# Kernel tuning notes

Hardware: AMD Instinct MI355X
Metric: run time of the kernel (lower is better)

Reference implementation:

```python
import jax, jax.numpy as jnp
import numpy as np

B, L, H, Dh, M = 4, 2048, 16, 256, 1024
D = H * Dh  # 4096

def setup_inputs() -> dict:
    key = jax.random.key(0)
    kx, ku, kd, kp = jax.random.split(key, 4)
    x = jax.random.normal(kx, (B, L, D), dtype=jnp.float32)
    up = jax.random.normal(ku, (H, Dh, M), dtype=jnp.float32)
    down = jax.random.normal(kd, (H, M, Dh), dtype=jnp.float32)
    perm = jax.random.permutation(kp, D)  # int32/int64 permutation of feature dim
    return {"x": x, "up": up, "down": down, "perm": perm}

def reference(x, up, down, perm):
    b, l, Dm = x.shape
    h, d = up.shape[0], up.shape[1]
    unperm = jnp.argsort(perm)  # inverse permutation (Unpermute buffer)
    t = x.reshape(b * l, Dm)
    t = t[:, perm]                     # PermuteIn gather
    t = t.reshape(b * l, h, d)
    t = jnp.einsum('bhd,hdm->bhm', t, up)      # per-head up-proj (grouped GEMM)
    t = jax.nn.gelu(t, approximate=False)      # nn.GELU default = exact erf
    t = jnp.einsum('bhm,hmd->bhd', t, down)    # per-head down-proj
    t = t.reshape(b * l, h * d)
    t = t[:, unperm]                   # Unpermute gather
    out = t.reshape(b, l, Dm)
    # residual=False: self.residual(x, residual) returns x (computed output)
    return out
```

## Files before the change

### kernel.cpp

```cpp
#include <hip/hip_runtime.h>
#include <hip/hip_bf16.h>
#include <math.h>


typedef __attribute__((ext_vector_type(8))) short bf16x8;
typedef __attribute__((ext_vector_type(4))) float f32x4;

__device__ __forceinline__ unsigned short f2bf(float f) {
    unsigned int u = __builtin_bit_cast(unsigned int, f);
    u = (u + 0x7FFFu + ((u >> 16) & 1u)) >> 16;
    return (unsigned short)u;
}
__device__ __forceinline__ float bf2f(unsigned short u) {
    return __builtin_bit_cast(float, ((unsigned int)u) << 16);
}

__device__ __forceinline__ float gelu_fast(float x) {
    float x2 = x * x;
    float a = x * __builtin_fmaf(-0.10294437f, x2, -2.3022082f);
    return x * __builtin_amdgcn_rcpf(1.0f + __builtin_amdgcn_exp2f(a));
}

__global__ __launch_bounds__(256) void transpose_cvt_kernel(
        const float* __restrict__ src, unsigned short* __restrict__ dst,
        int R, int C) {
    int tilesC = C >> 6;
    int tiles = tilesC * (R >> 6);
    int h = blockIdx.x / tiles;
    int t = blockIdx.x % tiles;
    int r0 = (t / tilesC) << 6;
    int c0 = (t % tilesC) << 6;
    const float* s = src + (size_t)h * R * C;
    unsigned short* d = dst + (size_t)h * R * C;
    __shared__ float tl[64][65];
    int col = threadIdx.x & 63;
    int rr = threadIdx.x >> 6;
    #pragma unroll
    for (int i = 0; i < 16; ++i) {
        int row = (i << 2) + rr;
        tl[row][col] = s[(size_t)(r0 + row) * C + (c0 + col)];
    }
    __syncthreads();
    #pragma unroll
    for (int i = 0; i < 16; ++i) {
        int row = (i << 2) + rr;
        d[(size_t)(c0 + row) * R + (r0 + col)] = f2bf(tl[col][row]);
    }
}

__global__ __launch_bounds__(256) void permute_x_kernel(
        const float* __restrict__ x, const int* __restrict__ perm,
        unsigned short* __restrict__ xP) {
    __shared__ unsigned short rbf[4][4096];
    __shared__ int sperm[4096];
    int tid = threadIdx.x;
    #pragma unroll
    for (int i = 0; i < 16; ++i) sperm[(i << 8) + tid] = perm[(i << 8) + tid];
    size_t r0 = (size_t)blockIdx.x << 2;
    #pragma unroll
    for (int rr = 0; rr < 4; ++rr) {
        const float4* xr = (const float4*)(x + ((r0 + rr) << 12));
        #pragma unroll
        for (int i = 0; i < 4; ++i) {
            float4 v = xr[(i << 8) + tid];
            int j = ((i << 8) + tid) << 2;
            uint2 wv;
            wv.x = f2bf(v.x) | ((unsigned int)f2bf(v.y) << 16);
            wv.y = f2bf(v.z) | ((unsigned int)f2bf(v.w) << 16);
            *(uint2*)(&rbf[rr][j]) = wv;
        }
    }
    __syncthreads();
    #pragma unroll
    for (int rr = 0; rr < 4; ++rr) {
        alignas(16) unsigned short tmp[16];
        int j0 = tid << 4;
        #pragma unroll
        for (int i = 0; i < 16; ++i) tmp[i] = rbf[rr][sperm[j0 + i]];
        *(uint4*)(xP + ((r0 + rr) << 12) + j0) = *(const uint4*)tmp;
        *(uint4*)(xP + ((r0 + rr) << 12) + j0 + 8) = *(const uint4*)(tmp + 8);
    }
}

template<int F32>
__global__ __launch_bounds__(256) void unpermute_kernel(
        const void* __restrict__ yPv, const int* __restrict__ perm,
        float* __restrict__ out) {
    __shared__ float rows[4][4096];
    __shared__ int sperm[4096];
    int tid = threadIdx.x;
    #pragma unroll
    for (int i = 0; i < 16; ++i) sperm[(i << 8) + tid] = perm[(i << 8) + tid];
    size_t r0 = (size_t)blockIdx.x << 2;
    int j0 = tid << 4;
    float vals[4][16];
    #pragma unroll
    for (int rr = 0; rr < 4; ++rr) {
        if (F32) {
            const float4* yr = (const float4*)((const float*)yPv + ((r0 + rr) << 12) + j0);
            #pragma unroll
            for (int i = 0; i < 4; ++i) {
                float4 v = yr[i];
                vals[rr][4 * i] = v.x; vals[rr][4 * i + 1] = v.y;
                vals[rr][4 * i + 2] = v.z; vals[rr][4 * i + 3] = v.w;
            }
        } else {
            const uint2* yr = (const uint2*)((const unsigned short*)yPv + ((r0 + rr) << 12) + j0);
            #pragma unroll
            for (int i = 0; i < 4; ++i) {
                uint2 v = yr[i];
                vals[rr][4 * i]     = bf2f((unsigned short)(v.x & 0xffffu));
                vals[rr][4 * i + 1] = bf2f((unsigned short)(v.x >> 16));
                vals[rr][4 * i + 2] = bf2f((unsigned short)(v.y & 0xffffu));
                vals[rr][4 * i + 3] = bf2f((unsigned short)(v.y >> 16));
            }
        }
    }
    __syncthreads();
    #pragma unroll
    for (int rr = 0; rr < 4; ++rr)
        #pragma unroll
        for (int i = 0; i < 16; ++i)
            rows[rr][sperm[j0 + i]] = vals[rr][i];
    __syncthreads();
    #pragma unroll
    for (int rr = 0; rr < 4; ++rr) {
        float4* orow = (float4*)(out + ((r0 + rr) << 12));
        #pragma unroll
        for (int i = 0; i < 4; ++i)
            orow[(i << 8) + tid] = *(const float4*)(&rows[rr][((i << 8) + tid) << 2]);
    }
}

template<int YPF32>
__global__ __launch_bounds__(256, 3) void ffn_kernel(
    const unsigned short* __restrict__ xP,
    const unsigned short* __restrict__ upT,
    const unsigned short* __restrict__ downT,
    void* __restrict__ yPv)
{
    __shared__ unsigned char sA[64 * 512];
    __shared__ unsigned char sH[64 * 256];

    int tid = threadIdx.x;
    int lane = tid & 63;
    int wave = tid >> 6;
    int l15 = lane & 15;
    int lq = lane >> 4;

    int bid = blockIdx.x;
    int nb = ((bid & 7) << 8) + (bid >> 3);
    int head = nb >> 7;
    int row0 = (nb & 127) << 6;

    #pragma unroll
    for (int i = 0; i < 8; ++i) {
        int idx = tid + (i << 8);
        int r = idx >> 5;
        int s = idx & 31;
        const unsigned short* src = xP + (((size_t)(row0 + r)) << 12) + (head << 8) + (s << 3);
        bf16x8 v = *(const bf16x8*)src;
        *(bf16x8*)(sA + r * 512 + ((s ^ (r & 31)) << 4)) = v;
    }
    __syncthreads();

    int wr = wave & 1;
    int wm = wave >> 1;

    f32x4 acc[4][4] = {};

    for (int mc = 0; mc < 8; ++mc) {
        int m0 = mc << 7;

        f32x4 hacc[4][2] = {};
        #pragma unroll
        for (int ks = 0; ks < 8; ++ks) {
            bf16x8 xb[2];
            #pragma unroll
            for (int j = 0; j < 2; ++j) {
                int r = ((2 * wr + j) << 4) + l15;
                int bo = r * 512 + ((((ks << 6) + (lq << 4))) ^ ((r & 31) << 4));
                xb[j] = *(const bf16x8*)(sA + bo);
            }
            bf16x8 wf[4];
            int kk = (ks << 5) + (lq << 3);
            #pragma unroll
            for (int i = 0; i < 4; ++i) {
                int m = m0 + (((wm << 2) + i) << 4) + l15;
                wf[i] = *(const bf16x8*)(upT + ((size_t)((head << 10) + m) << 8) + kk);
            }
            __builtin_amdgcn_s_setprio(1);
            #pragma unroll
            for (int i = 0; i < 4; ++i)
                #pragma unroll
                for (int j = 0; j < 2; ++j)
                    hacc[i][j] = __builtin_amdgcn_mfma_f32_16x16x32_bf16(wf[i], xb[j], hacc[i][j], 0, 0, 0);
            __builtin_amdgcn_s_setprio(0);
        }
        #pragma unroll
        for (int i = 0; i < 4; ++i) {
            #pragma unroll
            for (int j = 0; j < 2; ++j) {
                int r = ((2 * wr + j) << 4) + l15;
                int mbyte = (((wm << 2) + i) << 5) + (lq << 3);
                float g0 = gelu_fast(hacc[i][j][0]);
                float g1 = gelu_fast(hacc[i][j][1]);
                float g2 = gelu_fast(hacc[i][j][2]);
                float g3 = gelu_fast(hacc[i][j][3]);
                uint2 wv;
                wv.x = f2bf(g0) | ((unsigned int)f2bf(g1) << 16);
                wv.y = f2bf(g2) | ((unsigned int)f2bf(g3) << 16);
                *(uint2*)(sH + r * 256 + (mbyte ^ ((r & 15) << 4))) = wv;
            }
        }
        __syncthreads();

        #pragma unroll
        for (int ks = 0; ks < 4; ++ks) {
            bf16x8 ha[4];
            #pragma unroll
            for (int rb = 0; rb < 4; ++rb) {
                int r = (rb << 4) + l15;
                int bo = r * 256 + ((((ks << 6) + (lq << 4))) ^ ((r & 15) << 4));
                ha[rb] = *(const bf16x8*)(sH + bo);
            }
            bf16x8 wf[4];
            int mg = m0 + (ks << 5) + (lq << 3);
            #pragma unroll
            for (int i = 0; i < 4; ++i) {
                int d = (((wave << 2) + i) << 4) + l15;
                wf[i] = *(const bf16x8*)(downT + ((size_t)((head << 8) + d) << 10) + mg);
            }
            __builtin_amdgcn_s_setprio(1);
            #pragma unroll
            for (int i = 0; i < 4; ++i)
                #pragma unroll
                for (int rb = 0; rb < 4; ++rb)
                    acc[rb][i] = __builtin_amdgcn_mfma_f32_16x16x32_bf16(ha[rb], wf[i], acc[rb][i], 0, 0, 0);
            __builtin_amdgcn_s_setprio(0);
        }
        __syncthreads();
    }

    if (YPF32) {
        float* yp = (float*)yPv;
        #pragma unroll
        for (int rb = 0; rb < 4; ++rb)
            #pragma unroll
            for (int i = 0; i < 4; ++i) {
                int rg = row0 + (rb << 4) + (lq << 2);
                int dc = (head << 8) + (((wave << 2) + i) << 4) + l15;
                #pragma unroll
                for (int e = 0; e < 4; ++e)
                    yp[((size_t)(rg + e) << 12) + dc] = acc[rb][i][e];
            }
    } else {
        unsigned short* yp = (unsigned short*)yPv;
        #pragma unroll
        for (int rb = 0; rb < 4; ++rb)
            #pragma unroll
            for (int i = 0; i < 4; ++i) {
                int rg = row0 + (rb << 4) + (lq << 2);
                int dc = (head << 8) + (((wave << 2) + i) << 4) + l15;
                #pragma unroll
                for (int e = 0; e < 4; ++e)
                    yp[((size_t)(rg + e) << 12) + dc] = f2bf(acc[rb][i][e]);
            }
    }
}

extern "C" void kernel_launch(void* const* d_in, const int* in_sizes, int n_in,
                              void* d_out, int out_size, void* d_ws, size_t ws_size,
                              hipStream_t stream) {
    const float* x    = (const float*)d_in[0];
    const float* up   = (const float*)d_in[1];
    const float* down = (const float*)d_in[2];
    const int*   perm = (const int*)d_in[3];
    float* out = (float*)d_out;

    const size_t W = (size_t)16 * 1024 * 256;
    const size_t XN = (size_t)8192 * 4096;
    unsigned short* upT   = (unsigned short*)d_ws;
    unsigned short* downT = upT + W;
    unsigned short* xP    = downT + W;
    void* yP = (void*)(xP + XN);
    size_t base_bytes = (2 * W + XN) * 2;
    bool ypf32 = ws_size >= base_bytes + XN * 4;

    transpose_cvt_kernel<<<16 * 4 * 16, 256, 0, stream>>>(up, upT, 256, 1024);
    transpose_cvt_kernel<<<16 * 16 * 4, 256, 0, stream>>>(down, downT, 1024, 256);
    permute_x_kernel<<<2048, 256, 0, stream>>>(x, perm, xP);

    if (ypf32) {
        ffn_kernel<1><<<2048, 256, 0, stream>>>(xP, upT, downT, yP);
        unpermute_kernel<1><<<2048, 256, 0, stream>>>(yP, perm, out);
    } else {
        ffn_kernel<0><<<2048, 256, 0, stream>>>(xP, upT, downT, yP);
        unpermute_kernel<0><<<2048, 256, 0, stream>>>(yP, perm, out);
    }
}
```

Baseline: 659.2 us.

## Register-prefetch up/down weight fragments and reassign waves to full row set

Reworks the fused up-proj/GELU/down-proj kernel so each wave computes 32 M-columns across all 64 rows instead of a 2x2 row/column split. This halves the global up-weight fragment loads per wave while doubling LDS reads of the activation tile. It also software-pipelines the global weight loads for both GEMMs, loading the next k-step's fragments into registers before issuing the current MFMAs, including across chunk boundaries and before the barrier. The aim is to hide global load latency behind MFMA work, at the cost of more live registers and possibly lower occupancy.

```diff
diff --git a/kernel.cpp b/kernel.cpp
--- a/kernel.cpp
+++ b/kernel.cpp
@@ -153,6 +153,9 @@
     int head = nb >> 7;
     int row0 = (nb & 127) << 6;
 
+    const unsigned short* upH = upT + ((size_t)head << 18);
+    const unsigned short* dnH = downT + ((size_t)head << 18);
+
     #pragma unroll
     for (int i = 0; i < 8; ++i) {
         int idx = tid + (i << 8);
@@ -164,55 +167,73 @@
     }
     __syncthreads();
 
-    int wr = wave & 1;
-    int wm = wave >> 1;
+    int mrow0 = (wave << 5) + l15;
+    int kk0 = lq << 3;
 
     f32x4 acc[4][4] = {};
+
+    bf16x8 w1n0, w1n1;
+    {
+        const unsigned short* p = upH + (size_t)mrow0 * 256 + kk0;
+        w1n0 = *(const bf16x8*)p;
+        w1n1 = *(const bf16x8*)(p + 16 * 256);
+    }
 
     for (int mc = 0; mc < 8; ++mc) {
         int m0 = mc << 7;
 
-        f32x4 hacc[4][2] = {};
+        f32x4 hacc[2][4] = {};
         #pragma unroll
         for (int ks = 0; ks < 8; ++ks) {
-            bf16x8 xb[2];
-            #pragma unroll
-            for (int j = 0; j < 2; ++j) {
-                int r = ((2 * wr + j) << 4) + l15;
-                int bo = r * 512 + ((((ks << 6) + (lq << 4))) ^ ((r & 31) << 4));
-                xb[j] = *(const bf16x8*)(sA + bo);
-            }
-            bf16x8 wf[4];
-            int kk = (ks << 5) + (lq << 3);
-            #pragma unroll
-            for (int i = 0; i < 4; ++i) {
-                int m = m0 + (((wm << 2) + i) << 4) + l15;
-                wf[i] = *(const bf16x8*)(upT + ((size_t)((head << 10) + m) << 8) + kk);
+            bf16x8 w1c0 = w1n0, w1c1 = w1n1;
+            {
+                int nks = (ks + 1) & 7;
+                int nm0 = (ks == 7) ? (((mc + 1) & 7) << 7) : m0;
+                const unsigned short* p = upH + (size_t)(nm0 + mrow0) * 256 + (nks << 5) + kk0;
+                w1n0 = *(const bf16x8*)p;
+                w1n1 = *(const bf16x8*)(p + 16 * 256);
+            }
+            bf16x8 xb[4];
+            #pragma unroll
+            for (int rb = 0; rb < 4; ++rb) {
+                int r = (rb << 4) + l15;
+                xb[rb] = *(const bf16x8*)(sA + r * 512 + (((ks << 6) + (lq << 4)) ^ ((r & 31) << 4)));
             }
             __builtin_amdgcn_s_setprio(1);
             #pragma unroll
-            for (int i = 0; i < 4; ++i)
-                #pragma unroll
-                for (int j = 0; j < 2; ++j)
-                    hacc[i][j] = __builtin_amdgcn_mfma_f32_16x16x32_bf16(wf[i], xb[j], hacc[i][j], 0, 0, 0);
+            for (int rb = 0; rb < 4; ++rb) {
+                hacc[0][rb] = __builtin_amdgcn_mfma_f32_16x16x32_bf16(w1c0, xb[rb], hacc[0][rb], 0, 0, 0);
+                hacc[1][rb] = __builtin_amdgcn_mfma_f32_16x16x32_bf16(w1c1, xb[rb], hacc[1][rb], 0, 0, 0);
+            }
             __builtin_amdgcn_s_setprio(0);
         }
-        #pragma unroll
-        for (int i = 0; i < 4; ++i) {
-            #pragma unroll
-            for (int j = 0; j < 2; ++j) {
-                int r = ((2 * wr + j) << 4) + l15;
-                int mbyte = (((wm << 2) + i) << 5) + (lq << 3);
-                float g0 = gelu_fast(hacc[i][j][0]);
-                float g1 = gelu_fast(hacc[i][j][1]);
-                float g2 = gelu_fast(hacc[i][j][2]);
-                float g3 = gelu_fast(hacc[i][j][3]);
+
+        #pragma unroll
+        for (int jm = 0; jm < 2; ++jm) {
+            int mbyte = (((wave << 1) + jm) << 5) + (lq << 3);
+            #pragma unroll
+            for (int rb = 0; rb < 4; ++rb) {
+                int r = (rb << 4) + l15;
+                float g0 = gelu_fast(hacc[jm][rb][0]);
+                float g1 = gelu_fast(hacc[jm][rb][1]);
+                float g2 = gelu_fast(hacc[jm][rb][2]);
+                float g3 = gelu_fast(hacc[jm][rb][3]);
                 uint2 wv;
                 wv.x = f2bf(g0) | ((unsigned int)f2bf(g1) << 16);
                 wv.y = f2bf(g2) | ((unsigned int)f2bf(g3) << 16);
                 *(uint2*)(sH + r * 256 + (mbyte ^ ((r & 15) << 4))) = wv;
             }
         }
+
+        bf16x8 wf2[4];
+        {
+            int mg = m0 + kk0;
+            #pragma unroll
+            for (int i = 0; i < 4; ++i) {
+                int d = (((wave << 2) + i) << 4) + l15;
+                wf2[i] = *(const bf16x8*)(dnH + (size_t)d * 1024 + mg);
+            }
+        }
         __syncthreads();
 
         #pragma unroll
@@ -221,22 +242,25 @@
             #pragma unroll
             for (int rb = 0; rb < 4; ++rb) {
                 int r = (rb << 4) + l15;
-                int bo = r * 256 + ((((ks << 6) + (lq << 4))) ^ ((r & 15) << 4));
-                ha[rb] = *(const bf16x8*)(sH + bo);
-            }
-            bf16x8 wf[4];
-            int mg = m0 + (ks << 5) + (lq << 3);
-            #pragma unroll
-            for (int i = 0; i < 4; ++i) {
-                int d = (((wave << 2) + i) << 4) + l15;
-                wf[i] = *(const bf16x8*)(downT + ((size_t)((head << 8) + d) << 10) + mg);
+                ha[rb] = *(const bf16x8*)(sH + r * 256 + (((ks << 6) + (lq << 4)) ^ ((r & 15) << 4)));
+            }
+            bf16x8 wcur[4];
+            #pragma unroll
+            for (int i = 0; i < 4; ++i) wcur[i] = wf2[i];
+            if (ks < 3) {
+                int mg = m0 + ((ks + 1) << 5) + kk0;
+                #pragma unroll
+                for (int i = 0; i < 4; ++i) {
+                    int d = (((wave << 2) + i) << 4) + l15;
+                    wf2[i] = *(const bf16x8*)(dnH + (size_t)d * 1024 + mg);
+                }
             }
             __builtin_amdgcn_s_setprio(1);
             #pragma unroll
             for (int i = 0; i < 4; ++i)
                 #pragma unroll
                 for (int rb = 0; rb < 4; ++rb)
-                    acc[rb][i] = __builtin_amdgcn_mfma_f32_16x16x32_bf16(ha[rb], wf[i], acc[rb][i], 0, 0, 0);
+                    acc[rb][i] = __builtin_amdgcn_mfma_f32_16x16x32_bf16(ha[rb], wcur[i], acc[rb][i], 0, 0, 0);
             __builtin_amdgcn_s_setprio(0);
         }
         __syncthreads();
```

New measurement: 561.9 us. -14.8%, faster.
